# Performance work log

Measured on AMD Instinct MI355X. Metric: run time of the kernel, lower is better.

The kernel has to match this reference:

```python
import jax, jax.numpy as jnp
import numpy as np

B, N, EDGES = 16, 50000, 1600000
CLAMP_MIN, CLAMP_MAX = -10.0, 10.0
EPS = 1e-6


def setup_inputs() -> dict:
    key = jax.random.key(0)
    ks = jax.random.split(key, 8)
    return {
        "chem_influence": jax.random.normal(ks[0], (B, N), dtype=jnp.float32),
        "E": jax.random.normal(ks[1], (B, N), dtype=jnp.float32),
        "o_pre": jax.random.uniform(ks[2], (B, N), dtype=jnp.float32),
        "w": jax.random.normal(ks[3], (EDGES,), dtype=jnp.float32),
        "threshold": jax.random.uniform(ks[4], (N,), dtype=jnp.float32),
        "decay": jax.random.uniform(ks[5], (N,), dtype=jnp.float32),
        "src": jax.random.randint(ks[6], (EDGES,), 0, N, dtype=jnp.int32),
        "dst": jax.random.randint(ks[7], (EDGES,), 0, N, dtype=jnp.int32),
    }


def reference(chem_influence, E, o_pre, w, threshold, decay, src, dst):
    # Gap-junction currents: gather, sign-compare, weighted scatter-add.
    Oj = o_pre[:, src]                      # (B, EDGES) presynaptic outputs
    En = E[:, dst]                          # (B, EDGES) postsynaptic internal states
    sgn = jnp.where(Oj >= En, 1.0, -1.0)
    contrib = Oj * w * sgn                  # (B, EDGES)
    gj_sum = jnp.zeros_like(chem_influence).at[:, dst].add(contrib)  # (B, N)

    # Neuron dynamics (eqs 10, 11).
    S = jnp.clip(E + chem_influence + gj_sum, CLAMP_MIN, CLAMP_MAX)
    gt = S > threshold                      # broadcast (N,) over (B, N)
    mask = (~gt) & (jnp.abs(S - E) <= EPS)
    new_o = jax.nn.relu(S - threshold)
    new_e = jnp.where(gt, new_o, jnp.where(mask, E - decay, S))
    return (new_o, new_e)
```

## Files before the change

### kernel.cpp

```cpp
#include <hip/hip_runtime.h>

#define BATCH 16
#define NNODES 50000
#define NEDGES 1600000
#define BN (BATCH * NNODES)
#define CLAMP_LO -10.0f
#define CLAMP_HI 10.0f
#define EPS_V 1e-6f

#define NBINS 782
#define BSZ 64
#define CAPE 2560
#define K1B 250
#define EPS 6400
#define E4PS 1600
#define NPT 200
#define HROW 784

__global__ __launch_bounds__(256) void slice_sort(
    const float* __restrict__ o_pre, const float* __restrict__ E,
    const int* __restrict__ src, const int* __restrict__ dst,
    const float* __restrict__ w,
    float* __restrict__ o_t, float* __restrict__ E_t,
    int* __restrict__ hist,
    uint2* __restrict__ binned) {
    __shared__ int lh[NBINS];
    __shared__ int cur[NBINS];
    __shared__ int sm[256];
    const int tid = threadIdx.x, bid = blockIdx.x;

    for (int i = tid; i < NBINS; i += 256) lh[i] = 0;

    if (tid < NPT) {
        int t = bid * NPT + tid;
        float v[BATCH], u[BATCH];
#pragma unroll
        for (int b = 0; b < BATCH; ++b) {
            v[b] = o_pre[b * NNODES + t];
            u[b] = E[b * NNODES + t];
        }
        float4* op = (float4*)(o_t + (size_t)t * BATCH);
        float4* ep = (float4*)(E_t + (size_t)t * BATCH);
#pragma unroll
        for (int k = 0; k < 4; ++k) {
            op[k] = make_float4(v[4 * k], v[4 * k + 1], v[4 * k + 2], v[4 * k + 3]);
            ep[k] = make_float4(u[4 * k], u[4 * k + 1], u[4 * k + 2], u[4 * k + 3]);
        }
    }
    __syncthreads();

    const int4* dst4 = (const int4*)dst;
    const int i40 = bid * E4PS;
#pragma unroll
    for (int j = 0; j < 7; ++j) {
        int idx = j * 256 + tid;
        if (idx < E4PS) {
            int4 d4 = dst4[i40 + idx];
            atomicAdd(&lh[d4.x >> 6], 1);
            atomicAdd(&lh[d4.y >> 6], 1);
            atomicAdd(&lh[d4.z >> 6], 1);
            atomicAdd(&lh[d4.w >> 6], 1);
        }
    }
    __syncthreads();

    {
        int base = tid * 4;
        int v[4], psum = 0;
#pragma unroll
        for (int j = 0; j < 4; ++j) {
            int idx = base + j;
            v[j] = (idx < NBINS) ? lh[idx] : 0;
            psum += v[j];
        }
        sm[tid] = psum;
        __syncthreads();
        for (int off = 1; off < 256; off <<= 1) {
            int a = (tid >= off) ? sm[tid - off] : 0;
            __syncthreads();
            sm[tid] += a;
            __syncthreads();
        }
        int run = (tid > 0) ? sm[tid - 1] : 0;
#pragma unroll
        for (int j = 0; j < 4; ++j) {
            int idx = base + j;
            if (idx < NBINS + 1) {
                hist[(size_t)bid * HROW + idx] = run;
                if (idx < NBINS) cur[idx] = run;
            }
            if (idx < NBINS) run += v[j];
        }
    }
    __syncthreads();

    const int4*   src4 = (const int4*)src;
    const float4* w4   = (const float4*)w;
    uint2* out = binned + (size_t)bid * EPS;
#pragma unroll
    for (int j = 0; j < 7; ++j) {
        int idx = j * 256 + tid;
        if (idx < E4PS) {
            int4 d4 = dst4[i40 + idx];
            int4 s4 = src4[i40 + idx];
            float4 ww = w4[i40 + idx];
            int dd[4] = {d4.x, d4.y, d4.z, d4.w};
            int ss[4] = {s4.x, s4.y, s4.z, s4.w};
            float wv[4] = {ww.x, ww.y, ww.z, ww.w};
#pragma unroll
            for (int m = 0; m < 4; ++m) {
                int d = dd[m];
                int pos = atomicAdd(&cur[d >> 6], 1);
                out[pos] = make_uint2(
                    (unsigned)ss[m] | ((unsigned)(d & 63) << 16),
                    __float_as_uint(wv[m]));
            }
        }
    }
}

__global__ __launch_bounds__(256) void bin_gather3(
    const float* __restrict__ o_t, const float* __restrict__ E_t,
    const float* __restrict__ chem, const float* __restrict__ threshold,
    const float* __restrict__ decay, const int* __restrict__ hist,
    const uint2* __restrict__ binned,
    float* __restrict__ out_o, float* __restrict__ out_e) {
    __shared__ int   cnt_l[BSZ];
    __shared__ int   offs[BSZ + 1];
    __shared__ int   sc[BSZ];
    __shared__ uint2 eb[CAPE];

    const int k = blockIdx.x, tid = threadIdx.x;
    const int node0 = k * BSZ;
    const int nn = (NNODES - node0 < BSZ) ? (NNODES - node0) : BSZ;

    int st = 0, c = 0;
    if (tid < K1B) {
        st = hist[(size_t)tid * HROW + k];
        int en = hist[(size_t)tid * HROW + k + 1];
        c = en - st;
    }
    const uint2* sb = binned + (size_t)tid * EPS + st;

    if (tid < BSZ) cnt_l[tid] = 0;
    __syncthreads();
    for (int j = 0; j < c; ++j)
        atomicAdd(&cnt_l[(sb[j].x >> 16) & 63], 1);
    __syncthreads();

    if (tid < BSZ) sc[tid] = cnt_l[tid];
    __syncthreads();
    for (int o = 1; o < BSZ; o <<= 1) {
        int v = (tid >= o && tid < BSZ) ? sc[tid - o] : 0;
        __syncthreads();
        if (tid < BSZ) sc[tid] += v;
        __syncthreads();
    }
    if (tid < BSZ) {
        int ex = sc[tid] - cnt_l[tid];
        offs[tid] = ex;
        cnt_l[tid] = ex;
    }
    if (tid == 0) offs[BSZ] = sc[BSZ - 1];
    __syncthreads();

    for (int j = 0; j < c; ++j) {
        uint2 p = sb[j];
        int pos = atomicAdd(&cnt_l[(p.x >> 16) & 63], 1);
        if (pos < CAPE) eb[pos] = p;
    }
    __syncthreads();

    if (tid < nn * 4) {
        int n = tid >> 2;
        int q = (tid & 3) * 4;
        int gn = node0 + n;
        int e0 = offs[n], e1 = offs[n + 1];
        if (e1 > CAPE) e1 = CAPE;
        float4 en = *(const float4*)(E_t + (size_t)gn * BATCH + q);
        float4 acc = make_float4(0.f, 0.f, 0.f, 0.f);
        for (int i = e0; i < e1; ++i) {
            uint2 p = eb[i];
            float wv = __uint_as_float(p.y);
            int s = (int)(p.x & 0xFFFFu);
            float4 oj = *(const float4*)(o_t + (size_t)s * BATCH + q);
            acc.x += (oj.x >= en.x) ? oj.x * wv : -oj.x * wv;
            acc.y += (oj.y >= en.y) ? oj.y * wv : -oj.y * wv;
            acc.z += (oj.z >= en.z) ? oj.z * wv : -oj.z * wv;
            acc.w += (oj.w >= en.w) ? oj.w * wv : -oj.w * wv;
        }
        float th = threshold[gn];
        float dc = decay[gn];
        float ev[4] = {en.x, en.y, en.z, en.w};
        float av[4] = {acc.x, acc.y, acc.z, acc.w};
#pragma unroll
        for (int j = 0; j < 4; ++j) {
            int b = q + j;
            float e = ev[j];
            float S = e + chem[b * NNODES + gn] + av[j];
            S = fminf(fmaxf(S, CLAMP_LO), CLAMP_HI);
            float no = fmaxf(S - th, 0.0f);
            float ne;
            if (S > th) ne = no;
            else if (fabsf(S - e) <= EPS_V) ne = e - dc;
            else ne = S;
            out_o[b * NNODES + gn] = no;
            out_e[b * NNODES + gn] = ne;
        }
    }
}

__global__ void edge_scatter_dev(const float* __restrict__ o_pre, const float* __restrict__ E,
                                 const float* __restrict__ w, const int* __restrict__ src,
                                 const int* __restrict__ dst, float* __restrict__ gj) {
    int e = blockIdx.x * blockDim.x + threadIdx.x;
    if (e >= NEDGES) return;
    int s = src[e];
    int d = dst[e];
    float wv = w[e];
#pragma unroll
    for (int b = 0; b < BATCH; ++b) {
        float oj = o_pre[b * NNODES + s];
        float en = E[b * NNODES + d];
        atomicAdd(&gj[b * NNODES + d], (oj >= en) ? oj * wv : -oj * wv);
    }
}

__global__ void finalize_dev(const float* __restrict__ chem, const float* __restrict__ E,
                             const float* __restrict__ threshold, const float* __restrict__ decay,
                             float* __restrict__ out_o, float* __restrict__ out_e_gj) {
    int i = blockIdx.x * blockDim.x + threadIdx.x;
    if (i >= BN) return;
    int n = i % NNODES;
    float e = E[i];
    float S = e + chem[i] + out_e_gj[i];
    S = fminf(fmaxf(S, CLAMP_LO), CLAMP_HI);
    float th = threshold[n];
    float no = fmaxf(S - th, 0.0f);
    float ne;
    if (S > th) ne = no;
    else if (fabsf(S - e) <= EPS_V) ne = e - decay[n];
    else ne = S;
    out_o[i] = no;
    out_e_gj[i] = ne;
}

extern "C" void kernel_launch(void* const* d_in, const int* in_sizes, int n_in,
                              void* d_out, int out_size, void* d_ws, size_t ws_size,
                              hipStream_t stream) {
    const float* chem      = (const float*)d_in[0];
    const float* E         = (const float*)d_in[1];
    const float* o_pre     = (const float*)d_in[2];
    const float* w         = (const float*)d_in[3];
    const float* threshold = (const float*)d_in[4];
    const float* decay     = (const float*)d_in[5];
    const int*   src       = (const int*)d_in[6];
    const int*   dst       = (const int*)d_in[7];

    float* out_o = (float*)d_out;
    float* out_e = (float*)d_out + BN;

    const size_t OT_OFF  = 0;
    const size_t ET_OFF  = 3200000;
    const size_t BIN_OFF = 6400000;
    const size_t H_OFF   = 19200000;
    const size_t need    = H_OFF + (size_t)K1B * HROW * sizeof(int);

    if (ws_size >= need) {
        char* ws = (char*)d_ws;
        float* o_t    = (float*)(ws + OT_OFF);
        float* E_t    = (float*)(ws + ET_OFF);
        uint2* binned = (uint2*)(ws + BIN_OFF);
        int*   hist   = (int*)(ws + H_OFF);

        slice_sort<<<K1B, 256, 0, stream>>>(o_pre, E, src, dst, w,
                                            o_t, E_t, hist, binned);
        bin_gather3<<<NBINS, 256, 0, stream>>>(o_t, E_t, chem, threshold, decay,
                                               hist, binned, out_o, out_e);
    } else {
        hipMemsetAsync(out_e, 0, (size_t)BN * sizeof(float), stream);
        edge_scatter_dev<<<(NEDGES + 255) / 256, 256, 0, stream>>>(o_pre, E, w, src, dst, out_e);
        finalize_dev<<<(BN + 255) / 256, 256, 0, stream>>>(chem, E, threshold, decay, out_o, out_e);
    }
}
```

Before: 145.0 us.

## Use 512-thread blocks, stage bin edges once in LDS, split batch over 8 lanes

Both kernels now launch with 512 threads. The gather kernel reads each slice's binned edges from global memory only once, copying them into a raw LDS buffer while counting; the old code read them twice. The local counting sort then runs from LDS in parallel across all threads. Each node is now handled by 8 lanes of 2 batches each instead of 4 lanes of 4, which doubles the gather parallelism but uses narrower float2 loads and doubles LDS use for edge buffers.

```diff
diff --git a/kernel.cpp b/kernel.cpp
--- a/kernel.cpp
+++ b/kernel.cpp
@@ -17,7 +17,7 @@
 #define NPT 200
 #define HROW 784
 
-__global__ __launch_bounds__(256) void slice_sort(
+__global__ __launch_bounds__(512) void slice_sort(
     const float* __restrict__ o_pre, const float* __restrict__ E,
     const int* __restrict__ src, const int* __restrict__ dst,
     const float* __restrict__ w,
@@ -26,10 +26,10 @@
     uint2* __restrict__ binned) {
     __shared__ int lh[NBINS];
     __shared__ int cur[NBINS];
-    __shared__ int sm[256];
+    __shared__ int sm[512];
     const int tid = threadIdx.x, bid = blockIdx.x;
 
-    for (int i = tid; i < NBINS; i += 256) lh[i] = 0;
+    for (int i = tid; i < NBINS; i += 512) lh[i] = 0;
 
     if (tid < NPT) {
         int t = bid * NPT + tid;
@@ -52,8 +52,8 @@
     const int4* dst4 = (const int4*)dst;
     const int i40 = bid * E4PS;
 #pragma unroll
-    for (int j = 0; j < 7; ++j) {
-        int idx = j * 256 + tid;
+    for (int j = 0; j < 4; ++j) {
+        int idx = j * 512 + tid;
         if (idx < E4PS) {
             int4 d4 = dst4[i40 + idx];
             atomicAdd(&lh[d4.x >> 6], 1);
@@ -65,17 +65,17 @@
     __syncthreads();
 
     {
-        int base = tid * 4;
-        int v[4], psum = 0;
-#pragma unroll
-        for (int j = 0; j < 4; ++j) {
+        int base = tid * 2;
+        int v[2], psum = 0;
+#pragma unroll
+        for (int j = 0; j < 2; ++j) {
             int idx = base + j;
             v[j] = (idx < NBINS) ? lh[idx] : 0;
             psum += v[j];
         }
         sm[tid] = psum;
         __syncthreads();
-        for (int off = 1; off < 256; off <<= 1) {
+        for (int off = 1; off < 512; off <<= 1) {
             int a = (tid >= off) ? sm[tid - off] : 0;
             __syncthreads();
             sm[tid] += a;
@@ -83,7 +83,7 @@
         }
         int run = (tid > 0) ? sm[tid - 1] : 0;
 #pragma unroll
-        for (int j = 0; j < 4; ++j) {
+        for (int j = 0; j < 2; ++j) {
             int idx = base + j;
             if (idx < NBINS + 1) {
                 hist[(size_t)bid * HROW + idx] = run;
@@ -98,8 +98,8 @@
     const float4* w4   = (const float4*)w;
     uint2* out = binned + (size_t)bid * EPS;
 #pragma unroll
-    for (int j = 0; j < 7; ++j) {
-        int idx = j * 256 + tid;
+    for (int j = 0; j < 4; ++j) {
+        int idx = j * 512 + tid;
         if (idx < E4PS) {
             int4 d4 = dst4[i40 + idx];
             int4 s4 = src4[i40 + idx];
@@ -119,7 +119,7 @@
     }
 }
 
-__global__ __launch_bounds__(256) void bin_gather3(
+__global__ __launch_bounds__(512) void bin_gather4(
     const float* __restrict__ o_t, const float* __restrict__ E_t,
     const float* __restrict__ chem, const float* __restrict__ threshold,
     const float* __restrict__ decay, const int* __restrict__ hist,
@@ -128,25 +128,35 @@
     __shared__ int   cnt_l[BSZ];
     __shared__ int   offs[BSZ + 1];
     __shared__ int   sc[BSZ];
-    __shared__ uint2 eb[CAPE];
+    __shared__ int   tot;
+    __shared__ uint2 eb_raw[CAPE];
+    __shared__ uint2 ebs[CAPE];
 
     const int k = blockIdx.x, tid = threadIdx.x;
     const int node0 = k * BSZ;
     const int nn = (NNODES - node0 < BSZ) ? (NNODES - node0) : BSZ;
 
-    int st = 0, c = 0;
+    if (tid == 0) tot = 0;
+    if (tid < BSZ) cnt_l[tid] = 0;
+    __syncthreads();
+
     if (tid < K1B) {
-        st = hist[(size_t)tid * HROW + k];
+        int st = hist[(size_t)tid * HROW + k];
         int en = hist[(size_t)tid * HROW + k + 1];
-        c = en - st;
-    }
-    const uint2* sb = binned + (size_t)tid * EPS + st;
-
-    if (tid < BSZ) cnt_l[tid] = 0;
-    __syncthreads();
-    for (int j = 0; j < c; ++j)
-        atomicAdd(&cnt_l[(sb[j].x >> 16) & 63], 1);
-    __syncthreads();
+        int c = en - st;
+        if (c > 0) {
+            int p0 = atomicAdd(&tot, c);
+            const uint2* sb = binned + (size_t)tid * EPS + st;
+            for (int j = 0; j < c; ++j) {
+                uint2 p = sb[j];
+                if (p0 + j < CAPE) eb_raw[p0 + j] = p;
+                atomicAdd(&cnt_l[(p.x >> 16) & 63], 1);
+            }
+        }
+    }
+    __syncthreads();
+    int total = tot;
+    if (total > CAPE) total = CAPE;
 
     if (tid < BSZ) sc[tid] = cnt_l[tid];
     __syncthreads();
@@ -164,38 +174,37 @@
     if (tid == 0) offs[BSZ] = sc[BSZ - 1];
     __syncthreads();
 
-    for (int j = 0; j < c; ++j) {
-        uint2 p = sb[j];
+    for (int i = tid; i < total; i += 512) {
+        uint2 p = eb_raw[i];
         int pos = atomicAdd(&cnt_l[(p.x >> 16) & 63], 1);
-        if (pos < CAPE) eb[pos] = p;
-    }
-    __syncthreads();
-
-    if (tid < nn * 4) {
-        int n = tid >> 2;
-        int q = (tid & 3) * 4;
+        if (pos < CAPE) ebs[pos] = p;
+    }
+    __syncthreads();
+
+    if (tid < nn * 8) {
+        int n = tid >> 3;
+        int b0 = (tid & 7) * 2;
         int gn = node0 + n;
         int e0 = offs[n], e1 = offs[n + 1];
         if (e1 > CAPE) e1 = CAPE;
-        float4 en = *(const float4*)(E_t + (size_t)gn * BATCH + q);
-        float4 acc = make_float4(0.f, 0.f, 0.f, 0.f);
+        float2 en2 = *(const float2*)(E_t + (size_t)gn * BATCH + b0);
+        float ax = 0.f, ay = 0.f;
+#pragma unroll 4
         for (int i = e0; i < e1; ++i) {
-            uint2 p = eb[i];
+            uint2 p = ebs[i];
             float wv = __uint_as_float(p.y);
             int s = (int)(p.x & 0xFFFFu);
-            float4 oj = *(const float4*)(o_t + (size_t)s * BATCH + q);
-            acc.x += (oj.x >= en.x) ? oj.x * wv : -oj.x * wv;
-            acc.y += (oj.y >= en.y) ? oj.y * wv : -oj.y * wv;
-            acc.z += (oj.z >= en.z) ? oj.z * wv : -oj.z * wv;
-            acc.w += (oj.w >= en.w) ? oj.w * wv : -oj.w * wv;
+            float2 oj = *(const float2*)(o_t + (size_t)s * BATCH + b0);
+            ax += (oj.x >= en2.x) ? oj.x * wv : -oj.x * wv;
+            ay += (oj.y >= en2.y) ? oj.y * wv : -oj.y * wv;
         }
         float th = threshold[gn];
         float dc = decay[gn];
-        float ev[4] = {en.x, en.y, en.z, en.w};
-        float av[4] = {acc.x, acc.y, acc.z, acc.w};
-#pragma unroll
-        for (int j = 0; j < 4; ++j) {
-            int b = q + j;
+        float ev[2] = {en2.x, en2.y};
+        float av[2] = {ax, ay};
+#pragma unroll
+        for (int j = 0; j < 2; ++j) {
+            int b = b0 + j;
             float e = ev[j];
             float S = e + chem[b * NNODES + gn] + av[j];
             S = fminf(fmaxf(S, CLAMP_LO), CLAMP_HI);
@@ -273,9 +282,9 @@
         uint2* binned = (uint2*)(ws + BIN_OFF);
         int*   hist   = (int*)(ws + H_OFF);
 
-        slice_sort<<<K1B, 256, 0, stream>>>(o_pre, E, src, dst, w,
+        slice_sort<<<K1B, 512, 0, stream>>>(o_pre, E, src, dst, w,
                                             o_t, E_t, hist, binned);
-        bin_gather3<<<NBINS, 256, 0, stream>>>(o_t, E_t, chem, threshold, decay,
+        bin_gather4<<<NBINS, 512, 0, stream>>>(o_t, E_t, chem, threshold, decay,
                                                hist, binned, out_o, out_e);
     } else {
         hipMemsetAsync(out_e, 0, (size_t)BN * sizeof(float), stream);
```

New measurement: 142.8 us. Within noise of the previous version (-1.5%).
